# Kernel optimization log

Measured on AMD Instinct MI355X. Metric: run time of the kernel, lower is better.

Reference implementation:

```python
import jax, jax.numpy as jnp
import numpy as np

B, IN_F, OUT_F, AGG = 1024, 256, 128, 4

def setup_inputs() -> dict:
    key = jax.random.key(0)
    k1, k2 = jax.random.split(key)
    m = jax.random.uniform(k1, (B, IN_F), dtype=jnp.float32)
    weight = jax.random.uniform(k2, (IN_F, OUT_F * AGG), dtype=jnp.float32)
    return {"m": m, "weight": weight, "agg_features": AGG}

def reference(m, weight, agg_features):
    # tropical (max-min) semiring matmul: [B, IN] x [IN, OUT*AGG] -> [B, OUT*AGG]
    z = jnp.max(jnp.minimum(m[:, :, None], weight[None, :, :]), axis=1)
    # max-pool over trailing agg groups -> [B, OUT]
    out = z.reshape(z.shape[0], -1, agg_features).max(axis=-1)
    return out
```

## Files before the change

### kernel.cpp

```cpp
#include <hip/hip_runtime.h>
#include <hip/hip_bf16.h>


#define B_DIM 1024
#define K_DIM 256
#define O_DIM 128


__global__ __launch_bounds__(256) void agg_fold_kernel(
    const float* __restrict__ w, float* __restrict__ wpk) {
  const int t = blockIdx.x * 256 + threadIdx.x;
  const int k = t >> 7;
  const int o = t & 127;
  const float4 v = *(const float4*)(w + (size_t)k * 512 + o * 4);
  const float mx = fmaxf(fmaxf(v.x, v.y), fmaxf(v.z, v.w));
  wpk[((k >> 2) * O_DIM + o) * 4 + (k & 3)] = mx;
}

__global__ __launch_bounds__(256) void tropical_kernel(
    const float* __restrict__ m, const float* __restrict__ wpk,
    float* __restrict__ out) {
  const int tid = threadIdx.x;
  const int o = tid & 127;
  const int ty = tid >> 7;
  int b0 = blockIdx.x * 4 + ty * 2;
  b0 = __builtin_amdgcn_readfirstlane(b0);

  const float* mr0 = m + (size_t)b0 * K_DIM;
  const float* mr1 = mr0 + K_DIM;
  const float* wp = wpk + o * 4;

  float acc0 = -3.402823466e38f;
  float acc1 = -3.402823466e38f;

#pragma unroll 4
  for (int k = 0; k < K_DIM; k += 8) {
    const float4 w0 = *(const float4*)(wp + (k >> 2) * (O_DIM * 4));
    const float4 w1 = *(const float4*)(wp + (k >> 2) * (O_DIM * 4) + O_DIM * 4);
    const float4 a0 = *(const float4*)(mr0 + k);
    const float4 a1 = *(const float4*)(mr0 + k + 4);
    const float4 c0 = *(const float4*)(mr1 + k);
    const float4 c1 = *(const float4*)(mr1 + k + 4);
    acc0 = fmaxf(acc0, fmaxf(fminf(a0.x, w0.x), fminf(a0.y, w0.y)));
    acc0 = fmaxf(acc0, fmaxf(fminf(a0.z, w0.z), fminf(a0.w, w0.w)));
    acc0 = fmaxf(acc0, fmaxf(fminf(a1.x, w1.x), fminf(a1.y, w1.y)));
    acc0 = fmaxf(acc0, fmaxf(fminf(a1.z, w1.z), fminf(a1.w, w1.w)));
    acc1 = fmaxf(acc1, fmaxf(fminf(c0.x, w0.x), fminf(c0.y, w0.y)));
    acc1 = fmaxf(acc1, fmaxf(fminf(c0.z, w0.z), fminf(c0.w, w0.w)));
    acc1 = fmaxf(acc1, fmaxf(fminf(c1.x, w1.x), fminf(c1.y, w1.y)));
    acc1 = fmaxf(acc1, fmaxf(fminf(c1.z, w1.z), fminf(c1.w, w1.w)));
  }

  out[(size_t)b0 * O_DIM + o] = acc0;
  out[(size_t)b0 * O_DIM + O_DIM + o] = acc1;
}

extern "C" void kernel_launch(void* const* d_in, const int* in_sizes, int n_in,
                              void* d_out, int out_size, void* d_ws, size_t ws_size,
                              hipStream_t stream) {
  const float* m = (const float*)d_in[0];
  const float* w = (const float*)d_in[1];
  float* wpk = (float*)d_ws;
  float* out = (float*)d_out;

  agg_fold_kernel<<<(K_DIM * O_DIM) / 256, 256, 0, stream>>>(w, wpk);

  tropical_kernel<<<B_DIM / 4, 256, 0, stream>>>(m, wpk, out);
}
```

Before: 66.16 us.

## Split K across half-blocks, compute four rows per thread, combine via LDS

Each thread now accumulates four batch rows over half of the K dimension instead of two rows over all of K, and the two halves are max-reduced through shared memory. This doubles reuse of each loaded weight vector and halves weight traffic per block. The cost is a block barrier and a small LDS exchange, plus more live registers.

```diff
diff --git a/kernel.cpp b/kernel.cpp
--- a/kernel.cpp
+++ b/kernel.cpp
@@ -5,7 +5,6 @@
 #define B_DIM 1024
 #define K_DIM 256
 #define O_DIM 128
-
 
 __global__ __launch_bounds__(256) void agg_fold_kernel(
     const float* __restrict__ w, float* __restrict__ wpk) {
@@ -17,42 +16,53 @@
   wpk[((k >> 2) * O_DIM + o) * 4 + (k & 3)] = mx;
 }
 
+#define NEG_INF (-3.402823466e38f)
+
 __global__ __launch_bounds__(256) void tropical_kernel(
     const float* __restrict__ m, const float* __restrict__ wpk,
     float* __restrict__ out) {
+  __shared__ float comb[O_DIM * 4];
+
   const int tid = threadIdx.x;
   const int o = tid & 127;
-  const int ty = tid >> 7;
-  int b0 = blockIdx.x * 4 + ty * 2;
+  const int kh = tid >> 7;
+  int b0 = blockIdx.x * 4;
   b0 = __builtin_amdgcn_readfirstlane(b0);
+  const int k0 = __builtin_amdgcn_readfirstlane(kh << 7);
 
-  const float* mr0 = m + (size_t)b0 * K_DIM;
-  const float* mr1 = mr0 + K_DIM;
-  const float* wp = wpk + o * 4;
+  const float* mrow = m + (size_t)b0 * K_DIM + k0;
+  const float* wp = wpk + (size_t)(k0 >> 2) * (O_DIM * 4) + o * 4;
 
-  float acc0 = -3.402823466e38f;
-  float acc1 = -3.402823466e38f;
+  float a0 = NEG_INF, a1 = NEG_INF, a2 = NEG_INF, a3 = NEG_INF;
 
 #pragma unroll 4
-  for (int k = 0; k < K_DIM; k += 8) {
-    const float4 w0 = *(const float4*)(wp + (k >> 2) * (O_DIM * 4));
-    const float4 w1 = *(const float4*)(wp + (k >> 2) * (O_DIM * 4) + O_DIM * 4);
-    const float4 a0 = *(const float4*)(mr0 + k);
-    const float4 a1 = *(const float4*)(mr0 + k + 4);
-    const float4 c0 = *(const float4*)(mr1 + k);
-    const float4 c1 = *(const float4*)(mr1 + k + 4);
-    acc0 = fmaxf(acc0, fmaxf(fminf(a0.x, w0.x), fminf(a0.y, w0.y)));
-    acc0 = fmaxf(acc0, fmaxf(fminf(a0.z, w0.z), fminf(a0.w, w0.w)));
-    acc0 = fmaxf(acc0, fmaxf(fminf(a1.x, w1.x), fminf(a1.y, w1.y)));
-    acc0 = fmaxf(acc0, fmaxf(fminf(a1.z, w1.z), fminf(a1.w, w1.w)));
-    acc1 = fmaxf(acc1, fmaxf(fminf(c0.x, w0.x), fminf(c0.y, w0.y)));
-    acc1 = fmaxf(acc1, fmaxf(fminf(c0.z, w0.z), fminf(c0.w, w0.w)));
-    acc1 = fmaxf(acc1, fmaxf(fminf(c1.x, w1.x), fminf(c1.y, w1.y)));
-    acc1 = fmaxf(acc1, fmaxf(fminf(c1.z, w1.z), fminf(c1.w, w1.w)));
+  for (int g = 0; g < 32; ++g) {
+    const float4 w = *(const float4*)(wp + g * (O_DIM * 4));
+    const float4 m0 = *(const float4*)(mrow + g * 4);
+    const float4 m1 = *(const float4*)(mrow + K_DIM + g * 4);
+    const float4 m2 = *(const float4*)(mrow + 2 * K_DIM + g * 4);
+    const float4 m3 = *(const float4*)(mrow + 3 * K_DIM + g * 4);
+    a0 = fmaxf(a0, fmaxf(fmaxf(fminf(m0.x, w.x), fminf(m0.y, w.y)),
+                         fmaxf(fminf(m0.z, w.z), fminf(m0.w, w.w))));
+    a1 = fmaxf(a1, fmaxf(fmaxf(fminf(m1.x, w.x), fminf(m1.y, w.y)),
+                         fmaxf(fminf(m1.z, w.z), fminf(m1.w, w.w))));
+    a2 = fmaxf(a2, fmaxf(fmaxf(fminf(m2.x, w.x), fminf(m2.y, w.y)),
+                         fmaxf(fminf(m2.z, w.z), fminf(m2.w, w.w))));
+    a3 = fmaxf(a3, fmaxf(fmaxf(fminf(m3.x, w.x), fminf(m3.y, w.y)),
+                         fmaxf(fminf(m3.z, w.z), fminf(m3.w, w.w))));
   }
 
-  out[(size_t)b0 * O_DIM + o] = acc0;
-  out[(size_t)b0 * O_DIM + O_DIM + o] = acc1;
+  if (kh) {
+    *(float4*)&comb[o * 4] = make_float4(a0, a1, a2, a3);
+  }
+  __syncthreads();
+  if (!kh) {
+    const float4 c = *(const float4*)&comb[o * 4];
+    out[(size_t)(b0 + 0) * O_DIM + o] = fmaxf(a0, c.x);
+    out[(size_t)(b0 + 1) * O_DIM + o] = fmaxf(a1, c.y);
+    out[(size_t)(b0 + 2) * O_DIM + o] = fmaxf(a2, c.z);
+    out[(size_t)(b0 + 3) * O_DIM + o] = fmaxf(a3, c.w);
+  }
 }
 
 extern "C" void kernel_launch(void* const* d_in, const int* in_sizes, int n_in,
@@ -64,6 +74,5 @@
   float* out = (float*)d_out;
 
   agg_fold_kernel<<<(K_DIM * O_DIM) / 256, 256, 0, stream>>>(w, wpk);
-
   tropical_kernel<<<B_DIM / 4, 256, 0, stream>>>(m, wpk, out);
 }
```

Result: faster. 64.33 us (-2.8%).
